# Kernel optimization log

Measured on AMD Instinct MI355X. Metric: run time of the kernel, lower is better.

The kernel has to match this reference:

```python
import jax, jax.numpy as jnp
import numpy as np

SR = 44100.0
J, Q = 12, 16
W0 = 2.0 * np.pi      # MorletWavelet.freq_to_w_at_s(1.0, s=1.0) -> w = 2*pi*f*s
N_SIG = 3.0           # wavelet support = +/- N_SIG standard deviations


def _make_wavelet_bank():
    """Morlet filter bank: J octaves, Q steps/octave, highest freq = nyquist.
    Returns centered, zero-padded real/imag filter stacks of shape (K, Lmax)."""
    dt = 1.0 / SR
    nyq = SR / 2.0
    wavelets = []
    for j in range(J):
        for q in range(Q):
            f = nyq / (2.0 ** (j + q / Q))
            s = 1.0 / f                      # center freq f = W0/(2*pi*s) = 1/s
            M = int(np.ceil(N_SIG * s * SR))  # half support in samples
            t = np.arange(-M, M + 1) * dt
            psi = (np.pi ** -0.25) / np.sqrt(s) \
                * np.exp(1j * W0 * t / s) * np.exp(-0.5 * (t / s) ** 2)
            psi = psi / np.sum(np.abs(psi))   # L1 normalization
            wavelets.append(psi.astype(np.complex64))
    Lmax = max(len(p) for p in wavelets)       # odd (2*M_max + 1)
    bank = np.zeros((len(wavelets), Lmax), np.complex64)
    for i, p in enumerate(wavelets):
        left = (Lmax - len(p)) // 2            # center-pad each wavelet
        bank[i, left:left + len(p)] = p
    return bank


def setup_inputs() -> dict:
    key = jax.random.key(0)
    x = jax.random.normal(key, (2, 1, 32768), dtype=jnp.float32)
    bank = _make_wavelet_bank()
    return {
        "x": x,
        "filt_real": jnp.asarray(bank.real, dtype=jnp.float32),
        "filt_imag": jnp.asarray(bank.imag, dtype=jnp.float32),
    }


def _scat1d(x, filt_real, filt_imag):
    # x: (B, 1, T); filters: (K, L) with L odd. Equivalent to the torch path:
    # pad input by L//2, cross-correlate (F.conv1d) with each complex wavelet,
    # take the modulus. Done via FFT (same math, efficient for ~47k-tap kernels).
    K, L = filt_real.shape
    B, C, T = x.shape  # C == 1 (squeeze_channels=True)
    P = L // 2
    xp = jnp.pad(x[:, 0, :], ((0, 0), (P, P)))       # (B, T + 2P)
    n_full = xp.shape[-1] + L - 1
    N = 1 << (n_full - 1).bit_length()               # next pow2 FFT size
    X = jnp.fft.rfft(xp, N)                          # (B, N//2+1)
    Gr = jnp.fft.rfft(filt_real[:, ::-1], N)         # flip -> corr via conv
    Gi = jnp.fft.rfft(filt_imag[:, ::-1], N)         # (K, N//2+1)
    lo = L - 1                                       # valid-corr offset
    yr = jnp.fft.irfft(X[:, None, :] * Gr[None], N)[..., lo:lo + T]
    yi = jnp.fft.irfft(X[:, None, :] * Gi[None], N)[..., lo:lo + T]
    return jnp.sqrt(yr * yr + yi * yi)               # (B, K, T) modulus


def reference(x, filt_real, filt_imag):
    return _scat1d(x, filt_real, filt_imag)
```

## Files before the change

kernel.cpp:

```cpp
#include <hip/hip_runtime.h>
#include <math.h>

#define T_LEN   32768
#define NK      192
#define NB      2
#define KDIR    48
#define MAXM    56

struct SParams {
  int m1e[144];
  int voff[144];
  int slot[144];
  int ab[9];
  int jb[10];
};

__device__ __forceinline__ int j2_of_q(int q) {
  return 4 + (q >= 5) + (q >= 10) + (q >= 15);
}

__global__ __launch_bounds__(256) void k_vtab(float* __restrict__ ws, SParams P) {
  int ki = blockIdx.y;
  int slotc = P.slot[ki];
  int M1e = P.m1e[ki];
  float* dst = ws + P.voff[ki];
  int nent = 2 * M1e + 2;
  int k = ki + 48;
  int j = k >> 4, q = k & 15;
  float sig = 2.f * exp2f((float)(16 * j + q) * 0.0625f);
  float s1 = sig * 0.86602540378f;
  float gc = -0.5f / (s1 * s1);
  float om = 6.28318530718f / sig;
  float norm = 1.f / (2.50662827463f * s1 * erff((float)M1e / (1.41421356237f * s1)));
  #pragma unroll
  for (int e0 = 0; e0 < 4; ++e0) {
    int e = blockIdx.x * 1024 + e0 * 256 + threadIdx.x;
    if (e >= slotc) continue;
    if (e >= nent) { dst[2 * e] = 0.f; dst[2 * e + 1] = 0.f; continue; }
    float mm = (float)(e - M1e);
    float g = __expf(gc * mm * mm) * norm;
    float sn, cs; __sincosf(om * mm, &sn, &cs);
    dst[2 * e] = g * cs;
    dst[2 * e + 1] = g * sn;
  }
}


template<int J, int G, int E>
__device__ __forceinline__ void deep_path(const float* __restrict__ x,
                                          float* __restrict__ ws, const SParams& P,
                                          int q, int tile, int tid,
                                          float* xs, float* red) {
  constexpr int d = 1 << J;
  constexpr int W = E + (G - 1) * d + 2;
  const int ki = 16 * (J - 3) + q;
  const int J2 = j2_of_q(q);
  const int M1e = P.m1e[ki];
  const int slot = P.slot[ki];
  const float* vt = ws + P.voff[ki];
  const int n0 = tile * G;
  const int ubase0 = (n0 - J2) * d - M1e;
  const float* xb0 = x;
  const float* xb1 = x + T_LEN;

  float acc[4 * G];
  #pragma unroll
  for (int i = 0; i < 4 * G; ++i) acc[i] = 0.f;

  for (int e0 = 0; e0 < slot; e0 += E) {
    int ub = ubase0 + e0;
    if (ub >= T_LEN || ub + W <= 0) continue;
    int Ech = slot - e0; if (Ech > E) Ech = E;
    int Wn = Ech + (G - 1) * d + 2;
    int Wh = (Wn + 1) >> 1;
    for (int i = tid; i < Wh; i += 256) {
      int u0 = ub + 2 * i;
      bool ok = (unsigned)u0 <= (unsigned)(T_LEN - 2);
      int uc = ok ? u0 : 0;
      float2 a = *(const float2*)(xb0 + uc);
      float2 b = *(const float2*)(xb1 + uc);
      float4 w;
      w.x = ok ? a.x : 0.f; w.y = ok ? b.x : 0.f;
      w.z = ok ? a.y : 0.f; w.w = ok ? b.y : 0.f;
      *(float4*)(xs + 4 * i) = w;
    }
    __syncthreads();
    int pend = Ech >> 9;
    const float4* xp0 = (const float4*)xs + tid;
    const float* vte = vt + 2 * e0 + 4 * tid;
    for (int ps = 0; ps < pend; ++ps) {
      float4 v = *(const float4*)(vte + (ps << 10));
      const float4* xp = xp0 + (ps << 8);
      #pragma unroll
      for (int g = 0; g < G; ++g) {
        float4 xv = xp[g * (d >> 1)];
        acc[4 * g + 0] += v.x * xv.x + v.z * xv.z;
        acc[4 * g + 1] += v.y * xv.x + v.w * xv.z;
        acc[4 * g + 2] += v.x * xv.y + v.z * xv.w;
        acc[4 * g + 3] += v.y * xv.y + v.w * xv.w;
      }
    }
    __syncthreads();
  }

  #pragma unroll
  for (int st = 1; st < 64; st <<= 1) {
    #pragma unroll
    for (int i = 0; i < 4 * G; ++i) acc[i] += __shfl_xor(acc[i], st, 64);
  }
  int wv = tid >> 6;
  if ((tid & 63) == 0) {
    #pragma unroll
    for (int gg = 0; gg < G; ++gg)
      *(float4*)(red + wv * 64 + 4 * gg) =
        make_float4(acc[4 * gg], acc[4 * gg + 1], acc[4 * gg + 2], acc[4 * gg + 3]);
  }
  __syncthreads();
  if (tid < 4 * G)
    red[256 + tid] = red[tid] + red[64 + tid] + red[128 + tid] + red[192 + tid];
  __syncthreads();
  if (tid < G) {
    int nidx = n0 + tid;
    int Ncu = (32767 >> J) + 17;
    if (nidx < Ncu) {
      float ar0 = red[256 + 4 * tid], ai0 = red[256 + 4 * tid + 1];
      float ar1 = red[256 + 4 * tid + 2], ai1 = red[256 + 4 * tid + 3];
      float ndf = (float)((nidx - J2) * d);
      float rev = ndf * exp2f(-(float)(16 * (J + 1) + q) * 0.0625f);
      rev -= floorf(rev);
      float sn, cs; __sincosf(rev * 6.28318530718f, &sn, &cs);
      float* ap = ws + P.ab[J - 3] + (q * 2) * Ncu * 2;
      *(float2*)(ap + 2 * nidx) = make_float2(ar0 * cs - ai0 * sn, ar0 * sn + ai0 * cs);
      *(float2*)(ap + 2 * (Ncu + nidx)) = make_float2(ar1 * cs - ai1 * sn, ar1 * sn + ai1 * cs);
    }
  }
}

template<int J, int TOUT>
__device__ __forceinline__ void small_path(const float* __restrict__ x,
                                           float* __restrict__ ws, const SParams& P,
                                           int q, int tile, int tid,
                                           float* xs, float* red) {
  constexpr int d = 1 << J;
  const int ki = 16 * (J - 3) + q;
  const int J2 = j2_of_q(q);
  const int M1e = P.m1e[ki];
  const int nent = 2 * M1e + 2;
  const float* vt = ws + P.voff[ki];
  const int Ncu = (32767 >> J) + 17;
  const int o0 = tile * TOUT;
  const int ub = (o0 - J2) * d - M1e;
  const int W = (TOUT - 1) * d + nent;
  const int PS = W + (((W - 1) >> J) << 1) + 4;
  const float* xb0 = x;
  const float* xb1 = x + T_LEN;
  for (int i = tid; i < W; i += 256) {
    int u = ub + i;
    bool ok = (unsigned)u < (unsigned)T_LEN;
    int uc = ok ? u : 0;
    float a = xb0[uc]; a = ok ? a : 0.f;
    float bv = xb1[uc]; bv = ok ? bv : 0.f;
    int ad = i + ((i >> J) << 1);
    xs[ad] = a; xs[PS + ad] = bv;
  }
  __syncthreads();
  int th = (TOUT == 128) ? tid : (tid & 127);
  int o = th & (TOUT - 1);
  int b = th / TOUT;
  int half = (TOUT == 64) ? (tid >> 7) : 0;
  int e_lo = 0, e_hi = nent;
  if (TOUT == 64) {
    int eh = (nent >> 2) << 1;
    if (half) e_lo = eh; else e_hi = eh;
  }
  const float* pl = xs + b * PS;
  int sb = o * d;
  float ar = 0.f, ai = 0.f;
  #pragma unroll 4
  for (int e = e_lo; e < e_hi; e += 2) {
    float4 v = *(const float4*)(vt + 2 * e);
    int s = sb + e;
    float2 xv = *(const float2*)(pl + s + ((s >> J) << 1));
    ar += v.x * xv.x + v.z * xv.y;
    ai += v.y * xv.x + v.w * xv.y;
  }
  if (TOUT == 64) {
    if (tid >= 128) { red[2 * (tid - 128)] = ar; red[2 * (tid - 128) + 1] = ai; }
    __syncthreads();
    if (tid < 128) { ar += red[2 * tid]; ai += red[2 * tid + 1]; }
  }
  if (half == 0 && o0 + o < Ncu && (TOUT == 128 || tid < 128)) {
    int nidx = o0 + o;
    float ndf = (float)((nidx - J2) * d);
    float rev = ndf * exp2f(-(float)(16 * (J + 1) + q) * 0.0625f);
    rev -= floorf(rev);
    float sn, cs; __sincosf(rev * 6.28318530718f, &sn, &cs);
    float* ap = ws + P.ab[J - 3] + (q * 2) * Ncu * 2;
    *(float2*)(ap + 2 * (b * Ncu + nidx)) = make_float2(ar * cs - ai * sn, ar * sn + ai * cs);
  }
}

__global__ __launch_bounds__(256) void k_s1(const float* __restrict__ x,
                                            float* __restrict__ ws, SParams P) {
  __shared__ __align__(16) float xs[12292];
  __shared__ __align__(16) float red[512];
  int bx = blockIdx.x, tid = threadIdx.x;
  int o = 0;
  #pragma unroll
  for (int t = 1; t < 9; ++t) if (bx >= P.jb[t]) o = t;
  int j = 11 - o;
  int rem = bx - P.jb[o];
  int tile = rem >> 4, q = rem & 15;
  switch (j) {
    case 11: deep_path<11, 2, 4096>(x, ws, P, q, tile, tid, xs, red); break;
    case 10: deep_path<10, 3, 3584>(x, ws, P, q, tile, tid, xs, red); break;
    case 9:  deep_path<9, 4, 4096>(x, ws, P, q, tile, tid, xs, red); break;
    case 8:  deep_path<8, 8, 4096>(x, ws, P, q, tile, tid, xs, red); break;
    case 7:  deep_path<7, 16, 4096>(x, ws, P, q, tile, tid, xs, red); break;
    case 6:  small_path<6, 64>(x, ws, P, q, tile, tid, xs, red); break;
    case 5:  small_path<5, 128>(x, ws, P, q, tile, tid, xs, red); break;
    case 4:  small_path<4, 128>(x, ws, P, q, tile, tid, xs, red); break;
    default: small_path<3, 128>(x, ws, P, q, tile, tid, xs, red); break;
  }
}

__global__ __launch_bounds__(256) void k_stage2(const float* __restrict__ ws,
                                                float* __restrict__ out, SParams P) {
  int k = KDIR + blockIdx.y;
  int j = k >> 4, q = k & 15;
  int d = 1 << j;
  int J2 = j2_of_q(q);
  float sig = 2.f * exp2f((float)(16 * j + q) * 0.0625f);
  float s2 = sig * 0.5f;
  int Ncu = (32767 >> j) + 17;
  const float* A0 = ws + P.ab[j - 3] + (q * 2) * Ncu * 2;
  const float* A1 = A0 + Ncu * 2;
  int t0 = blockIdx.x * 256 + threadIdx.x;
  int phi = t0 & (d - 1);
  int nb0 = t0 >> j;
  int step = 8192 >> j;
  int ntap = 2 * J2 + 1;
  float fd = (float)d;
  float inv2 = 1.f / (s2 * s2);
  float u0 = (float)(phi + J2 * d);
  float eg = __expf(-0.5f * u0 * u0 * inv2);
  float mf = __expf((fd * u0 - 0.5f * fd * fd) * inv2);
  float qf = __expf(-fd * fd * inv2);
  float Z = 0.f;
  float sr0 = 0.f, si0 = 0.f, sr1 = 0.f, si1 = 0.f;
  float sr2 = 0.f, si2 = 0.f, sr3 = 0.f, si3 = 0.f;
  float tr0 = 0.f, ti0 = 0.f, tr1 = 0.f, ti1 = 0.f;
  float tr2 = 0.f, ti2 = 0.f, tr3 = 0.f, ti3 = 0.f;
  const float* Ap0 = A0 + 2 * nb0;
  const float* Ap1 = A1 + 2 * nb0;
  for (int rr = 0; rr < ntap; ++rr) {
    float w = eg; eg *= mf; mf *= qf; Z += w;
    float2 a0 = *(const float2*)(Ap0 + 2 * rr);
    float2 a1 = *(const float2*)(Ap0 + 2 * (rr + step));
    float2 a2 = *(const float2*)(Ap0 + 2 * (rr + 2 * step));
    float2 a3 = *(const float2*)(Ap0 + 2 * (rr + 3 * step));
    float2 b0 = *(const float2*)(Ap1 + 2 * rr);
    float2 b1 = *(const float2*)(Ap1 + 2 * (rr + step));
    float2 b2 = *(const float2*)(Ap1 + 2 * (rr + 2 * step));
    float2 b3 = *(const float2*)(Ap1 + 2 * (rr + 3 * step));
    sr0 += w * a0.x; si0 += w * a0.y; sr1 += w * a1.x; si1 += w * a1.y;
    sr2 += w * a2.x; si2 += w * a2.y; sr3 += w * a3.x; si3 += w * a3.y;
    tr0 += w * b0.x; ti0 += w * b0.y; tr1 += w * b1.x; ti1 += w * b1.y;
    tr2 += w * b2.x; ti2 += w * b2.y; tr3 += w * b3.x; ti3 += w * b3.y;
  }
  float zi = 1.f / Z;
  size_t ob0 = (size_t)k * T_LEN + t0;
  size_t ob1 = (size_t)(NK + k) * T_LEN + t0;
  out[ob0]         = sqrtf(sr0 * sr0 + si0 * si0) * zi;
  out[ob0 + 8192]  = sqrtf(sr1 * sr1 + si1 * si1) * zi;
  out[ob0 + 16384] = sqrtf(sr2 * sr2 + si2 * si2) * zi;
  out[ob0 + 24576] = sqrtf(sr3 * sr3 + si3 * si3) * zi;
  out[ob1]         = sqrtf(tr0 * tr0 + ti0 * ti0) * zi;
  out[ob1 + 8192]  = sqrtf(tr1 * tr1 + ti1 * ti1) * zi;
  out[ob1 + 16384] = sqrtf(tr2 * tr2 + ti2 * ti2) * zi;
  out[ob1 + 24576] = sqrtf(tr3 * tr3 + ti3 * ti3) * zi;
}

__global__ __launch_bounds__(256) void k_direct(const float* __restrict__ x,
                                               const float* __restrict__ fr,
                                               const float* __restrict__ fi,
                                               float* __restrict__ out, int Lmax) {
  int k = blockIdx.y;
  int b = blockIdx.z;
  int t0 = blockIdx.x * 1024;
  int j = k >> 4, q = k & 15;
  int M = (int)ceil(6.0 * exp2((double)j + (double)q * 0.0625)) + 2;
  int P = Lmax >> 1;
  __shared__ __align__(16) float xs[1024 + 2 * MAXM + 4];
  __shared__ __align__(16) float frs[2 * MAXM + 4], fis[2 * MAXM + 4];
  int tid = threadIdx.x;
  int xlen = 1024 + 2 * M;
  const float* xb = x + b * T_LEN;
  for (int i = tid; i < xlen; i += 256) {
    int u = t0 - M + i;
    xs[i] = (u >= 0 && u < T_LEN) ? xb[u] : 0.f;
  }
  if (tid < 4) xs[xlen + tid] = 0.f;
  const float* frk = fr + (size_t)k * Lmax + (P - M);
  const float* fik = fi + (size_t)k * Lmax + (P - M);
  int tl = 2 * M + 1;
  for (int i = tid; i < tl; i += 256) { frs[i] = frk[i]; fis[i] = fik[i]; }
  if (tid < 3) { frs[tl + tid] = 0.f; fis[tl + tid] = 0.f; }
  __syncthreads();
  float ar0 = 0.f, ar1 = 0.f, ar2 = 0.f, ar3 = 0.f;
  float ai0 = 0.f, ai1 = 0.f, ai2 = 0.f, ai3 = 0.f;
  const float4* xsv = (const float4*)(xs + 4 * tid);
  float4 w0 = xsv[0];
  int groups = (tl + 3) >> 2;
  for (int g = 0; g < groups; ++g) {
    float4 w1 = xsv[g + 1];
    float4 f4 = *(const float4*)(frs + 4 * g);
    float4 h4 = *(const float4*)(fis + 4 * g);
    ar0 += f4.x * w0.x + f4.y * w0.y + f4.z * w0.z + f4.w * w0.w;
    ai0 += h4.x * w0.x + h4.y * w0.y + h4.z * w0.z + h4.w * w0.w;
    ar1 += f4.x * w0.y + f4.y * w0.z + f4.z * w0.w + f4.w * w1.x;
    ai1 += h4.x * w0.y + h4.y * w0.z + h4.z * w0.w + h4.w * w1.x;
    ar2 += f4.x * w0.z + f4.y * w0.w + f4.z * w1.x + f4.w * w1.y;
    ai2 += h4.x * w0.z + h4.y * w0.w + h4.z * w1.x + h4.w * w1.y;
    ar3 += f4.x * w0.w + f4.y * w1.x + f4.z * w1.y + f4.w * w1.z;
    ai3 += h4.x * w0.w + h4.y * w1.x + h4.z * w1.y + h4.w * w1.z;
    w0 = w1;
  }
  size_t ob = (size_t)(b * NK + k) * T_LEN + t0 + 4 * tid;
  float4 res;
  res.x = sqrtf(ar0 * ar0 + ai0 * ai0);
  res.y = sqrtf(ar1 * ar1 + ai1 * ai1);
  res.z = sqrtf(ar2 * ar2 + ai2 * ai2);
  res.w = sqrtf(ar3 * ar3 + ai3 * ai3);
  *(float4*)(out + ob) = res;
}

extern "C" void kernel_launch(void* const* d_in, const int* in_sizes, int n_in,
                              void* d_out, int out_size, void* d_ws, size_t ws_size,
                              hipStream_t stream) {
  const float* x  = (const float*)d_in[0];
  const float* fr = (const float*)d_in[1];
  const float* fi = (const float*)d_in[2];
  float* out = (float*)d_out;
  float* ws  = (float*)d_ws;
  int Lmax = in_sizes[1] / NK;

  SParams Pm;
  int cur = 0, maxslot = 0;
  for (int ki = 0; ki < 144; ++ki) {
    int j = (ki + 48) >> 4, q = ki & 15;
    double sig = 2.0 * exp2(((double)(16 * j + q)) / 16.0);
    double s1 = sig * 0.86602540378443864676;
    int M1 = (int)ceil(3.5 * s1);
    int M1e = (M1 + 1) & ~1;
    int slotc = (2 * M1e + 2 + 511) & ~511;
    Pm.m1e[ki] = M1e;
    Pm.voff[ki] = cur;
    Pm.slot[ki] = slotc;
    if (slotc > maxslot) maxslot = slotc;
    cur += 2 * slotc;
  }
  for (int j = 3; j <= 11; ++j) {
    Pm.ab[j - 3] = cur;
    cur += 32 * ((32767 >> j) + 17) * 2;
  }
  const int TO[9] = {2, 3, 4, 8, 16, 64, 128, 128, 128};
  Pm.jb[0] = 0;
  for (int o = 0; o < 9; ++o) {
    int j = 11 - o;
    int Ncu = (32767 >> j) + 17;
    int tiles = (Ncu + TO[o] - 1) / TO[o];
    Pm.jb[o + 1] = Pm.jb[o] + 16 * tiles;
  }

  k_vtab<<<dim3((maxslot + 1023) / 1024, 144), dim3(256), 0, stream>>>(ws, Pm);
  k_s1<<<dim3(Pm.jb[9]), dim3(256), 0, stream>>>(x, ws, Pm);
  k_direct<<<dim3(T_LEN / 1024, KDIR, NB), dim3(256), 0, stream>>>(x, fr, fi, out, Lmax);
  k_stage2<<<dim3(T_LEN / (256 * 4), NK - KDIR), dim3(256), 0, stream>>>(ws, out, Pm);
}
```

Measured before the change: 250.8 us.

## Split deep-octave filter taps across blocks with atomic accumulation

Splits the long filter-tap loop of the deepest octaves (j=9..11) into several chunks, each handled by its own block. The partial sums are combined with atomicAdd into a workspace region that a new kernel zeroes first. The aim is more parallelism, so that a few very long blocks do not leave the GPU underfilled. In exchange it adds a zeroing launch, atomic traffic and nondeterministic float summation order.

```diff
diff --git a/kernel.cpp b/kernel.cpp
--- a/kernel.cpp
+++ b/kernel.cpp
@@ -45,18 +45,28 @@
   }
 }
 
-
-template<int J, int G, int E>
+__global__ __launch_bounds__(256) void k_zero(float* __restrict__ ws, int base, int n) {
+  int i = blockIdx.x * 256 + threadIdx.x;
+  if (i < n) ws[base + i] = 0.f;
+}
+
+
+template<int J, int G, int S, int CH>
 __device__ __forceinline__ void deep_path(const float* __restrict__ x,
                                           float* __restrict__ ws, const SParams& P,
-                                          int q, int tile, int tid,
+                                          int q, int rc, int tid,
                                           float* xs, float* red) {
   constexpr int d = 1 << J;
+  constexpr int E = 4096;
   constexpr int W = E + (G - 1) * d + 2;
+  const int tile = rc / CH;
+  const int chunk = rc % CH;
   const int ki = 16 * (J - 3) + q;
   const int J2 = j2_of_q(q);
   const int M1e = P.m1e[ki];
   const int slot = P.slot[ki];
+  const int e_base = chunk * (S * E);
+  if (e_base >= slot) return;
   const float* vt = ws + P.voff[ki];
   const int n0 = tile * G;
   const int ubase0 = (n0 - J2) * d - M1e;
@@ -67,7 +77,10 @@
   #pragma unroll
   for (int i = 0; i < 4 * G; ++i) acc[i] = 0.f;
 
-  for (int e0 = 0; e0 < slot; e0 += E) {
+  #pragma unroll
+  for (int s = 0; s < S; ++s) {
+    int e0 = e_base + s * E;
+    if (e0 >= slot) break;
     int ub = ubase0 + e0;
     if (ub >= T_LEN || ub + W <= 0) continue;
     int Ech = slot - e0; if (Ech > E) Ech = E;
@@ -130,8 +143,17 @@
       rev -= floorf(rev);
       float sn, cs; __sincosf(rev * 6.28318530718f, &sn, &cs);
       float* ap = ws + P.ab[J - 3] + (q * 2) * Ncu * 2;
-      *(float2*)(ap + 2 * nidx) = make_float2(ar0 * cs - ai0 * sn, ar0 * sn + ai0 * cs);
-      *(float2*)(ap + 2 * (Ncu + nidx)) = make_float2(ar1 * cs - ai1 * sn, ar1 * sn + ai1 * cs);
+      float r0 = ar0 * cs - ai0 * sn, i0 = ar0 * sn + ai0 * cs;
+      float r1 = ar1 * cs - ai1 * sn, i1 = ar1 * sn + ai1 * cs;
+      if (CH == 1) {
+        *(float2*)(ap + 2 * nidx) = make_float2(r0, i0);
+        *(float2*)(ap + 2 * (Ncu + nidx)) = make_float2(r1, i1);
+      } else {
+        atomicAdd(ap + 2 * nidx, r0);
+        atomicAdd(ap + 2 * nidx + 1, i0);
+        atomicAdd(ap + 2 * (Ncu + nidx), r1);
+        atomicAdd(ap + 2 * (Ncu + nidx) + 1, i1);
+      }
     }
   }
 }
@@ -210,17 +232,17 @@
   for (int t = 1; t < 9; ++t) if (bx >= P.jb[t]) o = t;
   int j = 11 - o;
   int rem = bx - P.jb[o];
-  int tile = rem >> 4, q = rem & 15;
+  int rc = rem >> 4, q = rem & 15;
   switch (j) {
-    case 11: deep_path<11, 2, 4096>(x, ws, P, q, tile, tid, xs, red); break;
-    case 10: deep_path<10, 3, 3584>(x, ws, P, q, tile, tid, xs, red); break;
-    case 9:  deep_path<9, 4, 4096>(x, ws, P, q, tile, tid, xs, red); break;
-    case 8:  deep_path<8, 8, 4096>(x, ws, P, q, tile, tid, xs, red); break;
-    case 7:  deep_path<7, 16, 4096>(x, ws, P, q, tile, tid, xs, red); break;
-    case 6:  small_path<6, 64>(x, ws, P, q, tile, tid, xs, red); break;
-    case 5:  small_path<5, 128>(x, ws, P, q, tile, tid, xs, red); break;
-    case 4:  small_path<4, 128>(x, ws, P, q, tile, tid, xs, red); break;
-    default: small_path<3, 128>(x, ws, P, q, tile, tid, xs, red); break;
+    case 11: deep_path<11, 2, 2, 6>(x, ws, P, q, rc, tid, xs, red); break;
+    case 10: deep_path<10, 3, 2, 3>(x, ws, P, q, rc, tid, xs, red); break;
+    case 9:  deep_path<9, 4, 1, 3>(x, ws, P, q, rc, tid, xs, red); break;
+    case 8:  deep_path<8, 8, 2, 1>(x, ws, P, q, rc, tid, xs, red); break;
+    case 7:  deep_path<7, 16, 1, 1>(x, ws, P, q, rc, tid, xs, red); break;
+    case 6:  small_path<6, 64>(x, ws, P, q, rc, tid, xs, red); break;
+    case 5:  small_path<5, 128>(x, ws, P, q, rc, tid, xs, red); break;
+    case 4:  small_path<4, 128>(x, ws, P, q, rc, tid, xs, red); break;
+    default: small_path<3, 128>(x, ws, P, q, rc, tid, xs, red); break;
   }
 }
 
@@ -364,16 +386,27 @@
     Pm.ab[j - 3] = cur;
     cur += 32 * ((32767 >> j) + 17) * 2;
   }
-  const int TO[9] = {2, 3, 4, 8, 16, 64, 128, 128, 128};
+  const int DG[5]  = {2, 3, 4, 8, 16};
+  const int DCH[5] = {6, 3, 3, 1, 1};
   Pm.jb[0] = 0;
   for (int o = 0; o < 9; ++o) {
     int j = 11 - o;
     int Ncu = (32767 >> j) + 17;
-    int tiles = (Ncu + TO[o] - 1) / TO[o];
-    Pm.jb[o + 1] = Pm.jb[o] + 16 * tiles;
-  }
+    int cnt;
+    if (o < 5) {
+      int tiles = (Ncu + DG[o] - 1) / DG[o];
+      cnt = tiles * DCH[o] * 16;
+    } else {
+      int TOUT = (j == 6) ? 64 : 128;
+      cnt = ((Ncu + TOUT - 1) / TOUT) * 16;
+    }
+    Pm.jb[o + 1] = Pm.jb[o] + cnt;
+  }
+  int zbase = Pm.ab[6];
+  int zn = (Pm.ab[8] + 32 * ((32767 >> 11) + 17) * 2) - zbase;
 
   k_vtab<<<dim3((maxslot + 1023) / 1024, 144), dim3(256), 0, stream>>>(ws, Pm);
+  k_zero<<<dim3((zn + 255) / 256), dim3(256), 0, stream>>>(ws, zbase, zn);
   k_s1<<<dim3(Pm.jb[9]), dim3(256), 0, stream>>>(x, ws, Pm);
   k_direct<<<dim3(T_LEN / 1024, KDIR, NB), dim3(256), 0, stream>>>(x, fr, fi, out, Lmax);
   k_stage2<<<dim3(T_LEN / (256 * 4), NK - KDIR), dim3(256), 0, stream>>>(ws, out, Pm);
```

New measurement: 251.5 us. Within noise of the previous version (+0.3%).
